# Kernel optimization log

Measured on AMD Instinct MI355X. Metric: run time of the kernel, lower is better.

The kernel has to match this reference:

```python
import jax, jax.numpy as jnp
import numpy as np

B, L, T, V = 32, 200, 500, 80
DM, DE = 256, 512
D4 = 4 * DM              # 1024 (decoder LSTM width)
R = 2                    # reduction rate
STEPS = T // R           # 250 decoder steps
KSIZE, PADC, NFILT, DA = 31, 15, 32, 128
ZONEOUT, KEEP = 0.1, 0.5
MAXSTEP = 500            # hard-coded attention buffer length


def setup_inputs() -> dict:
    key = jax.random.key(0)
    ks = jax.random.split(key, 24)
    def lin(k, fan_in, shape):
        s = 1.0 / np.sqrt(fan_in)
        return jax.random.uniform(k, shape, minval=-s, maxval=s, dtype=jnp.float32)
    return {
        'meltarget': jax.random.normal(ks[0], (B, T, V), jnp.float32),
        'e_outputs': jax.random.normal(ks[1], (B, L, DE), jnp.float32),
        'conv_w':    lin(ks[2], KSIZE, (NFILT, 1, KSIZE)),
        'W_convproj': lin(ks[3], NFILT, (NFILT, DA)),
        'W_encproj': lin(ks[4], DE, (DE, DA)), 'b_encproj': lin(ks[5], DE, (DA,)),
        'W_decproj': lin(ks[6], D4, (D4, DA)),
        'W_self':    lin(ks[7], DA, (DA,)),
        'W_pre1': lin(ks[8], V, (V, DM)),   'b_pre1': lin(ks[9], V, (DM,)),
        'W_pre2': lin(ks[10], DM, (DM, DM)), 'b_pre2': lin(ks[11], DM, (DM,)),
        'W_l1_ys': lin(ks[12], DM, (DM, 4 * D4)),
        'W_l1_ss': lin(ks[13], D4, (D4, 4 * D4)),
        'W_l1_gs': lin(ks[14], 2 * DM, (2 * DM, 4 * D4)), 'b_l1_gs': lin(ks[15], 2 * DM, (4 * D4,)),
        'W_l2_is': lin(ks[16], D4, (D4, 4 * D4)),
        'W_l2_ss': lin(ks[17], D4, (D4, 4 * D4)), 'b_l2_ss': lin(ks[18], D4, (4 * D4,)),
        'W_frame': lin(ks[19], D4 + 2 * DM, (D4 + 2 * DM, V * R)), 'b_frame': lin(ks[20], D4 + 2 * DM, (V * R,)),
        'W_token': lin(ks[21], D4 + 2 * DM, (D4 + 2 * DM, R)),     'b_token': lin(ks[22], D4 + 2 * DM, (R,)),
    }


def _gate(x):
    # tanh(x*0.5)*0.5 + 0.5 == sigmoid(x), kept in the original's form
    return jnp.tanh(x * 0.5) * 0.5 + 0.5


def reference(meltarget, e_outputs, conv_w, W_convproj, W_encproj, b_encproj,
              W_decproj, W_self, W_pre1, b_pre1, W_pre2, b_pre2,
              W_l1_ys, W_l1_ss, W_l1_gs, b_l1_gs, W_l2_is, W_l2_ss, b_l2_ss,
              W_frame, b_frame, W_token, b_token):
    base_key = jax.random.key(1234)
    encproj = e_outputs @ W_encproj + b_encproj              # [B,L,DA], step-invariant
    mel_last = jnp.transpose(meltarget[:, R - 1::R, :], (1, 0, 2))  # [STEPS,B,V]

    def step_fn(carry, xs):
        prev_pred, cum_alpha, s1, c1, s2, c2 = carry
        step, mel_t = xs
        kd1, kd2, kz1, kz2 = jax.random.split(jax.random.fold_in(base_key, step), 4)
        # location-sensitive attention
        ac = jax.lax.conv_general_dilated(
            cum_alpha[:, None, :], conv_w, (1,), [(PADC, PADC)],
            dimension_numbers=('NCH', 'OIH', 'NCH'))         # [B,32,L]
        attconv = jnp.einsum('bfl,fa->bla', ac, W_convproj)  # [B,L,DA]
        decproj = (s2 @ W_decproj)[:, None, :]               # [B,1,DA]
        e = jnp.tanh(decproj + encproj + attconv)
        score = e @ W_self                                   # [B,L]
        alpha = jax.nn.softmax(score, axis=1)
        cum_alpha = cum_alpha + alpha
        g = jnp.einsum('bl,bld->bd', alpha, e_outputs)       # [B,DE]
        # prenet with dropout p=0.5
        pre1 = jax.nn.relu(prev_pred @ W_pre1 + b_pre1)
        pre1 = pre1 * jax.random.bernoulli(kd1, KEEP, pre1.shape) / KEEP
        pre2 = jax.nn.relu(pre1 @ W_pre2 + b_pre2)
        pre2 = pre2 * jax.random.bernoulli(kd2, KEEP, pre2.shape) / KEEP
        # LSTM cell 1 with zoneout
        rec = pre2 @ W_l1_ys + s1 @ W_l1_ss + g @ W_l1_gs + b_l1_gs
        i1, f1, cg1, o1 = jnp.split(rec, 4, axis=1)
        m1 = jnp.floor(jax.random.uniform(kz1, (B, D4)) + ZONEOUT)  # Bernoulli(zoneout) keep-old mask
        c1n = m1 * c1 + (1.0 - m1) * (_gate(f1) * c1 + _gate(i1) * jnp.tanh(cg1))
        s1n = m1 * s1 + (1.0 - m1) * (_gate(o1) * jnp.tanh(c1n))
        # LSTM cell 2 with zoneout
        rec2 = s1n @ W_l2_is + s2 @ W_l2_ss + b_l2_ss
        i2, f2, cg2, o2 = jnp.split(rec2, 4, axis=1)
        m2 = jnp.floor(jax.random.uniform(kz2, (B, D4)) + ZONEOUT)
        c2n = m2 * c2 + (1.0 - m2) * (_gate(f2) * c2 + _gate(i2) * jnp.tanh(cg2))
        s2n = m2 * s2 + (1.0 - m2) * (_gate(o2) * jnp.tanh(c2n))
        proj_in = jnp.concatenate([s2n, g], axis=1)          # [B, D4+2*DM]
        frame = proj_in @ W_frame + b_frame                  # [B, R*V]
        token = proj_in @ W_token + b_token                  # [B, R]
        return (mel_t, cum_alpha, s1n, c1n, s2n, c2n), (frame, token, alpha)

    z = jnp.zeros((B, D4), jnp.float32)
    carry0 = (jnp.zeros((B, V), jnp.float32), jnp.zeros((B, L), jnp.float32), z, z, z, z)
    _, (frames, tokens, alphas) = jax.lax.scan(step_fn, carry0, (jnp.arange(STEPS), mel_last))
    frame_sent = jnp.transpose(frames, (1, 0, 2)).reshape(B, STEPS * R, V)
    token_sent = jnp.transpose(tokens, (1, 0, 2)).reshape(B, STEPS * R)
    attn = jnp.zeros((B, MAXSTEP, L), jnp.float32).at[:, :STEPS].set(
        jax.lax.stop_gradient(jnp.transpose(alphas, (1, 0, 2))))
    return frame_sent, token_sent, attn
```

## Files before the change

### kernel.cpp

```cpp
#include <hip/hip_runtime.h>
#include <cstdint>
#include <cstddef>


static constexpr int NSTEP = 250;

static constexpr size_t OFF_ENCPROJ = 0;
static constexpr size_t OFF_CWT     = 819200;
static constexpr size_t OFF_KEYS    = 823296;
static constexpr size_t OFF_PRE2    = 825344;
static constexpr size_t OFF_G       = 2873344;
static constexpr size_t OFF_S2      = 6969344;
static constexpr size_t OFF_S1      = 15194112;
static constexpr size_t OFF_C1      = 15259648;
static constexpr size_t OFF_C2      = 15292416;
static constexpr size_t OFF_CUM     = 15325184;
static constexpr size_t OFF_DPART   = 15333376;
static constexpr size_t OFF_SC      = 15366144;
static constexpr size_t OFF_P1      = 15390720;
static constexpr size_t OFF_P2      = 17225728;

static constexpr size_t OUT_TOK  = 1280000;
static constexpr size_t OUT_ATTN = 1296000;

__device__ __forceinline__ uint2 threefry(unsigned k0, unsigned k1, unsigned c0, unsigned c1) {
  unsigned ks2 = k0 ^ k1 ^ 0x1BD11BDAu;
  unsigned x0 = c0 + k0, x1 = c1 + k1;
#define TFR(rot) { x0 += x1; x1 = (x1 << (rot)) | (x1 >> (32 - (rot))); x1 ^= x0; }
  TFR(13) TFR(15) TFR(26) TFR(6)   x0 += k1;  x1 += ks2 + 1u;
  TFR(17) TFR(29) TFR(16) TFR(24)  x0 += ks2; x1 += k0 + 2u;
  TFR(13) TFR(15) TFR(26) TFR(6)   x0 += k0;  x1 += k1 + 3u;
  TFR(17) TFR(29) TFR(16) TFR(24)  x0 += k1;  x1 += ks2 + 4u;
  TFR(13) TFR(15) TFR(26) TFR(6)   x0 += ks2; x1 += k0 + 5u;
#undef TFR
  return make_uint2(x0, x1);
}

__device__ __forceinline__ float u32_to_uniform(unsigned b) {
  return __uint_as_float((b >> 9) | 0x3f800000u) - 1.0f;
}

__device__ __forceinline__ float rng_uniform(unsigned k0, unsigned k1, unsigned i) {
  uint2 h = threefry(k0, k1, 0u, i);
  return u32_to_uniform(h.x ^ h.y);
}

__device__ __forceinline__ float gatef(float x) { return tanhf(x * 0.5f) * 0.5f + 0.5f; }

#define FMA4(A, S, W) { (A).x = fmaf((S), (W).x, (A).x); (A).y = fmaf((S), (W).y, (A).y); \
                        (A).z = fmaf((S), (W).z, (A).z); (A).w = fmaf((S), (W).w, (A).w); }

__global__ __launch_bounds__(256) void k_init(float* __restrict__ ws, float* __restrict__ out,
                                              const float* __restrict__ conv_w,
                                              const float* __restrict__ Wcp) {
  const size_t NZERO1 = 172032;
  const size_t NZERO2 = 32768;
  const size_t NATTN  = 1600000;
  const size_t NKEYS  = 250;
  const size_t NCWT   = 4096;
  const size_t TOTAL  = NZERO1 + NZERO2 + NATTN + NKEYS + NCWT;
  unsigned* keys = (unsigned*)(ws + OFF_KEYS);
  for (size_t i = (size_t)blockIdx.x * 256 + threadIdx.x; i < TOTAL; i += (size_t)gridDim.x * 256) {
    if (i < NZERO1) {
      ws[OFF_S1 + i] = 0.f;
    } else if (i < NZERO1 + NZERO2) {
      ws[OFF_S2 + (i - NZERO1)] = 0.f;
    } else if (i < NZERO1 + NZERO2 + NATTN) {
      size_t r = i - NZERO1 - NZERO2;
      size_t b = r / 50000, rem = r % 50000;
      out[OUT_ATTN + b * 100000 + 50000 + rem] = 0.f;
    } else if (i < NZERO1 + NZERO2 + NATTN + NKEYS) {
      int s = (int)(i - NZERO1 - NZERO2 - NATTN);
      uint2 F = threefry(0u, 1234u, 0u, (unsigned)s);
      uint2 kd1 = threefry(F.x, F.y, 0u, 0u);
      uint2 kd2 = threefry(F.x, F.y, 0u, 1u);
      uint2 kz1 = threefry(F.x, F.y, 0u, 2u);
      uint2 kz2 = threefry(F.x, F.y, 0u, 3u);
      keys[s * 8 + 0] = kd1.x; keys[s * 8 + 1] = kd1.y;
      keys[s * 8 + 2] = kd2.x; keys[s * 8 + 3] = kd2.y;
      keys[s * 8 + 4] = kz1.x; keys[s * 8 + 5] = kz1.y;
      keys[s * 8 + 6] = kz2.x; keys[s * 8 + 7] = kz2.y;
    } else {
      size_t r = i - NZERO1 - NZERO2 - NATTN - NKEYS;
      int a = (int)(r >> 5), kk = (int)(r & 31);
      float v = 0.f;
      if (kk < 31) {
        for (int f = 0; f < 32; ++f) v = fmaf(conv_w[f * 31 + kk], Wcp[f * 128 + a], v);
      }
      ws[OFF_CWT + r] = v;
    }
  }
}

__global__ __launch_bounds__(256) void k_encproj(const float* __restrict__ e_out,
                                                 const float* __restrict__ Wenc,
                                                 const float* __restrict__ benc,
                                                 float* __restrict__ encproj) {
  __shared__ __align__(16) float xs[32 * 516];
  int t = threadIdx.x;
  int r0 = blockIdx.x * 32;
  for (int i = 0; i < 64; ++i) {
    int idx = t + 256 * i; int rb = idx >> 9, kk = idx & 511;
    xs[rb * 516 + kk] = e_out[(size_t)(r0 + rb) * 512 + kk];
  }
  __syncthreads();
  int a = t & 127, rh = t >> 7;
  float acc[16];
#pragma unroll
  for (int r = 0; r < 16; ++r) acc[r] = 0.f;
  const float4* xv = (const float4*)xs;
  for (int k4 = 0; k4 < 128; ++k4) {
    const float* wp = Wenc + (size_t)(k4 * 4) * 128 + a;
    float w0 = wp[0], w1 = wp[128], w2 = wp[256], w3 = wp[384];
#pragma unroll
    for (int r = 0; r < 16; ++r) {
      float4 x4 = xv[(rh * 16 + r) * 129 + k4];
      acc[r] = fmaf(x4.x, w0, acc[r]); acc[r] = fmaf(x4.y, w1, acc[r]);
      acc[r] = fmaf(x4.z, w2, acc[r]); acc[r] = fmaf(x4.w, w3, acc[r]);
    }
  }
  float bb = benc[a];
  for (int r = 0; r < 16; ++r)
    encproj[(size_t)(r0 + rh * 16 + r) * 128 + a] = acc[r] + bb;
}

__global__ __launch_bounds__(256) void k_prenet(const float* __restrict__ mel,
                                                const float* __restrict__ W1, const float* __restrict__ b1,
                                                const float* __restrict__ W2, const float* __restrict__ b2,
                                                const unsigned* __restrict__ keys,
                                                float* __restrict__ pre2_all) {
  int s = blockIdx.x, t = threadIdx.x;
  __shared__ __align__(16) float prev[32 * 80];
  __shared__ __align__(16) float p1[32 * 256];
  for (int i = 0; i < 10; ++i) {
    int idx = t + 256 * i;
    int bb = idx / 80, vv = idx % 80;
    prev[idx] = (s == 0) ? 0.f : mel[(size_t)bb * 40000 + (size_t)(2 * s - 1) * 80 + vv];
  }
  __syncthreads();
  unsigned kd10 = keys[s * 8 + 0], kd11 = keys[s * 8 + 1];
  unsigned kd20 = keys[s * 8 + 2], kd21 = keys[s * 8 + 3];
  float acc[32];
  float bias = b1[t];
#pragma unroll
  for (int b = 0; b < 32; ++b) acc[b] = bias;
  for (int k4 = 0; k4 < 20; ++k4) {
    const float* wp = W1 + (size_t)(k4 * 4) * 256 + t;
    float w0 = wp[0], w1 = wp[256], w2 = wp[512], w3 = wp[768];
#pragma unroll
    for (int b = 0; b < 32; ++b) {
      float4 x4 = *(const float4*)(prev + b * 80 + k4 * 4);
      acc[b] = fmaf(x4.x, w0, acc[b]); acc[b] = fmaf(x4.y, w1, acc[b]);
      acc[b] = fmaf(x4.z, w2, acc[b]); acc[b] = fmaf(x4.w, w3, acc[b]);
    }
  }
#pragma unroll
  for (int b = 0; b < 32; ++b) {
    float r = fmaxf(acc[b], 0.f);
    float u = rng_uniform(kd10, kd11, (unsigned)(b * 256 + t));
    p1[b * 256 + t] = (u < 0.5f) ? r * 2.f : 0.f;
  }
  __syncthreads();
  float bias2 = b2[t];
#pragma unroll
  for (int b = 0; b < 32; ++b) acc[b] = bias2;
  for (int k4 = 0; k4 < 64; ++k4) {
    const float* wp = W2 + (size_t)(k4 * 4) * 256 + t;
    float w0 = wp[0], w1 = wp[256], w2 = wp[512], w3 = wp[768];
#pragma unroll
    for (int b = 0; b < 32; ++b) {
      float4 x4 = *(const float4*)(p1 + b * 256 + k4 * 4);
      acc[b] = fmaf(x4.x, w0, acc[b]); acc[b] = fmaf(x4.y, w1, acc[b]);
      acc[b] = fmaf(x4.z, w2, acc[b]); acc[b] = fmaf(x4.w, w3, acc[b]);
    }
  }
  for (int b = 0; b < 32; ++b) {
    float r = fmaxf(acc[b], 0.f);
    float u = rng_uniform(kd20, kd21, (unsigned)(b * 256 + t));
    pre2_all[(size_t)(s * 32 + b) * 256 + t] = (u < 0.5f) ? r * 2.f : 0.f;
  }
}

__global__ __launch_bounds__(256) void k_escore(const float* __restrict__ dpart,
                                                const float* __restrict__ encproj,
                                                const float* __restrict__ cwt,
                                                const float* __restrict__ cum,
                                                const float* __restrict__ Wself,
                                                float* __restrict__ sglob) {
  int b = blockIdx.x & 31, p = blockIdx.x >> 5;
  int t = threadIdx.x;
  __shared__ float dp[128];
  __shared__ float ca[232];
  __shared__ float scpart[4];
  if (t < 128) {
    float acc = 0.f;
#pragma unroll
    for (int q = 0; q < 8; ++q) acc += dpart[(b * 8 + q) * 128 + t];
    dp[t] = acc;
  }
  if (t < 232) ca[t] = (t >= 15 && t < 215) ? cum[b * 200 + (t - 15)] : 0.f;
  __syncthreads();
  int a = t & 127, lh = t >> 7;
  float cwr[31];
#pragma unroll
  for (int k = 0; k < 31; ++k) cwr[k] = cwt[a * 32 + k];
  float wself = Wself[a];
  float dpr = dp[a];
  for (int ii = 0; ii < 13; ++ii) {
    int lo = ii * 2 + lh;
    int l = p * 25 + lo;
    float v = 0.f;
    if (lo < 25) {
      float conv = 0.f;
#pragma unroll
      for (int k = 0; k < 31; ++k) conv = fmaf(ca[l + k], cwr[k], conv);
      float e = tanhf(dpr + encproj[(size_t)(b * 200 + l) * 128 + a] + conv);
      v = e * wself;
    }
#pragma unroll
    for (int off = 32; off > 0; off >>= 1) v += __shfl_xor(v, off, 64);
    if ((t & 63) == 0) scpart[t >> 6] = v;
    __syncthreads();
    if (t == 0) sglob[b * 200 + p * 25 + ii * 2] = scpart[0] + scpart[1];
    if (t == 128 && ii < 12) sglob[b * 200 + p * 25 + ii * 2 + 1] = scpart[2] + scpart[3];
    __syncthreads();
  }
}

__global__ __launch_bounds__(256) void k_attng(const float* __restrict__ sglob,
                                               const float* __restrict__ e_out,
                                               float* __restrict__ cum,
                                               float* __restrict__ g_out,
                                               float* __restrict__ attn_out) {
  int b = blockIdx.x & 31, p = blockIdx.x >> 5;
  int t = threadIdx.x;
  __shared__ float sc[200];
  __shared__ float red[8];
  __shared__ float bcv[2];
  __shared__ float gpart[4][64];
  if (t < 200) sc[t] = sglob[b * 200 + t];
  __syncthreads();
  float v = (t < 200) ? sc[t] : -3.4e38f;
#pragma unroll
  for (int off = 32; off > 0; off >>= 1) v = fmaxf(v, __shfl_xor(v, off, 64));
  if ((t & 63) == 0) red[t >> 6] = v;
  __syncthreads();
  if (t == 0) bcv[0] = fmaxf(fmaxf(red[0], red[1]), fmaxf(red[2], red[3]));
  __syncthreads();
  float mx = bcv[0];
  float ex = (t < 200) ? expf(sc[t] - mx) : 0.f;
  float sv = ex;
#pragma unroll
  for (int off = 32; off > 0; off >>= 1) sv += __shfl_xor(sv, off, 64);
  if ((t & 63) == 0) red[4 + (t >> 6)] = sv;
  __syncthreads();
  if (t == 0) bcv[1] = (red[4] + red[5]) + (red[6] + red[7]);
  __syncthreads();
  float denom = bcv[1];
  if (t < 200) {
    float al = ex / denom;
    sc[t] = al;
    if (p == 0) {
      cum[b * 200 + t] += al;
      attn_out[(size_t)b * 100000 + t] = al;
    }
  }
  __syncthreads();
  int d = p * 64 + (t & 63), lq = t >> 6;
  const float* eb = e_out + (size_t)b * 102400 + d;
  float acc = 0.f;
  for (int l = lq * 50; l < lq * 50 + 50; ++l) acc = fmaf(sc[l], eb[(size_t)l * 512], acc);
  gpart[lq][t & 63] = acc;
  __syncthreads();
  if (t < 64)
    g_out[b * 512 + p * 64 + t] = (gpart[0][t] + gpart[1][t]) + (gpart[2][t] + gpart[3][t]);
}

__device__ __forceinline__ void gemm_body(
    const float* __restrict__ W0, int k0,
    float* __restrict__ part, int c, int jt,
    const float* __restrict__ xs ) {
  int t = threadIdx.x;
  int jq = t & 31, bq = t >> 5;
  int j = jt * 32 + jq;
  float4 acc[4];
  acc[0] = acc[1] = acc[2] = acc[3] = make_float4(0, 0, 0, 0);
  const float4* xv = (const float4*)xs;
  const float* Wb = W0 + (size_t)k0 * 4096 + j;
#pragma unroll 4
  for (int k4 = 0; k4 < 32; ++k4) {
    float4 xq[4];
    xq[0] = xv[(bq * 4 + 0) * 33 + k4];
    xq[1] = xv[(bq * 4 + 1) * 33 + k4];
    xq[2] = xv[(bq * 4 + 2) * 33 + k4];
    xq[3] = xv[(bq * 4 + 3) * 33 + k4];
    const float* wr = Wb + (size_t)(k4 * 4) * 4096;
#pragma unroll
    for (int ks = 0; ks < 4; ++ks) {
      float wi = wr[0], wf = wr[1024], wc = wr[2048], wo = wr[3072];
      wr += 4096;
#pragma unroll
      for (int r = 0; r < 4; ++r) {
        float xval = ((const float*)&xq[r])[ks];
        acc[r].x = fmaf(xval, wi, acc[r].x);
        acc[r].y = fmaf(xval, wf, acc[r].y);
        acc[r].z = fmaf(xval, wc, acc[r].z);
        acc[r].w = fmaf(xval, wo, acc[r].w);
      }
    }
  }
  float* pb = part + (size_t)c * 131072 + (size_t)(bq * 4) * 4096 + j;
#pragma unroll
  for (int r = 0; r < 4; ++r) {
    float* pr = pb + r * 4096;
    pr[0] = acc[r].x; pr[1024] = acc[r].y; pr[2048] = acc[r].z; pr[3072] = acc[r].w;
  }
}

__global__ __launch_bounds__(256) void k_b1g(
    const float* __restrict__ pre2_s, const float* __restrict__ s1old,
    const float* __restrict__ g_s,
    const float* __restrict__ Wys, const float* __restrict__ Wss, const float* __restrict__ Wgs,
    float* __restrict__ part) {
  int t = threadIdx.x;
  int jt = blockIdx.x & 31, c = blockIdx.x >> 5;
  __shared__ __align__(16) float xs[32 * 132];
  {
    int r = t >> 3, kq = t & 7;
    const float* src;
    if (c < 2)       src = pre2_s + r * 256 + c * 128;
    else if (c < 10) src = s1old + r * 1024 + (c - 2) * 128;
    else             src = g_s + r * 512 + (c - 10) * 128;
    const float4* s4 = (const float4*)(src + kq * 16);
    float4* d4 = (float4*)(xs + r * 132 + kq * 16);
    d4[0] = s4[0]; d4[1] = s4[1]; d4[2] = s4[2]; d4[3] = s4[3];
  }
  const float* W0; int k0;
  if (c < 2)       { W0 = Wys; k0 = c * 128; }
  else if (c < 10) { W0 = Wss; k0 = (c - 2) * 128; }
  else             { W0 = Wgs; k0 = (c - 10) * 128; }
  __syncthreads();
  gemm_body(W0, k0, part, c, jt, xs);
}

__global__ __launch_bounds__(256) void k_b2g(
    const float* __restrict__ s1new, const float* __restrict__ s2prev,
    const float* __restrict__ Wis, const float* __restrict__ Wss2,
    float* __restrict__ part) {
  int t = threadIdx.x;
  int jt = blockIdx.x & 31, c = blockIdx.x >> 5;
  __shared__ __align__(16) float xs[32 * 132];
  {
    int r = t >> 3, kq = t & 7;
    const float* src = (c < 8) ? (s1new + r * 1024 + c * 128)
                               : (s2prev + r * 1024 + (c - 8) * 128);
    const float4* s4 = (const float4*)(src + kq * 16);
    float4* d4 = (float4*)(xs + r * 132 + kq * 16);
    d4[0] = s4[0]; d4[1] = s4[1]; d4[2] = s4[2]; d4[3] = s4[3];
  }
  const float* W0; int k0;
  if (c < 8) { W0 = Wis;  k0 = c * 128; }
  else       { W0 = Wss2; k0 = (c - 8) * 128; }
  __syncthreads();
  gemm_body(W0, k0, part, c, jt, xs);
}

__global__ __launch_bounds__(256) void k_cell1(
    const float* __restrict__ part, const float* __restrict__ bias,
    const float* __restrict__ sold, float* __restrict__ snew, float* __restrict__ cst,
    const unsigned* __restrict__ keyp) {
  int e = blockIdx.x * 256 + threadIdx.x;
  int b = e >> 10, j = e & 1023;
  float gi = bias[j], gf = bias[1024 + j], gc = bias[2048 + j], go = bias[3072 + j];
  const float* pc = part + (size_t)b * 4096 + j;
#pragma unroll
  for (int cc = 0; cc < 14; ++cc) {
    const float* p2 = pc + (size_t)cc * 131072;
    gi += p2[0]; gf += p2[1024]; gc += p2[2048]; go += p2[3072];
  }
  float u = rng_uniform(keyp[0], keyp[1], (unsigned)e);
  float m = floorf(u + 0.1f);
  float co = cst[e], so = sold[e];
  float cn = fmaf(gatef(gf), co, gatef(gi) * tanhf(gc));
  float cnew = (m > 0.5f) ? co : cn;
  float sn = (m > 0.5f) ? so : (gatef(go) * tanhf(cnew));
  cst[e] = cnew;
  snew[e] = sn;
}

__global__ __launch_bounds__(256) void k_cell2dp(
    const float* __restrict__ part, const float* __restrict__ bias,
    const float* __restrict__ sold, float* __restrict__ snew, float* __restrict__ cst,
    const unsigned* __restrict__ keyp,
    const float* __restrict__ Wdec, float* __restrict__ dpart) {
  int b = blockIdx.x & 31, p = blockIdx.x >> 5;
  int t = threadIdx.x;
  __shared__ float s2l[128];
  __shared__ float dtmp[256];
  if (t < 128) {
    int j = p * 128 + t;
    int e = b * 1024 + j;
    float gi = bias[j], gf = bias[1024 + j], gc = bias[2048 + j], go = bias[3072 + j];
    const float* pc = part + (size_t)b * 4096 + j;
#pragma unroll
    for (int cc = 0; cc < 16; ++cc) {
      const float* p2 = pc + (size_t)cc * 131072;
      gi += p2[0]; gf += p2[1024]; gc += p2[2048]; go += p2[3072];
    }
    float u = rng_uniform(keyp[0], keyp[1], (unsigned)e);
    float m = floorf(u + 0.1f);
    float co = cst[e], so = sold[e];
    float cn = fmaf(gatef(gf), co, gatef(gi) * tanhf(gc));
    float cnew = (m > 0.5f) ? co : cn;
    float sn = (m > 0.5f) ? so : (gatef(go) * tanhf(cnew));
    cst[e] = cnew;
    snew[e] = sn;
    s2l[t] = sn;
  }
  __syncthreads();
  int a = t & 127, h = t >> 7;
  const float* wp = Wdec + (size_t)(p * 128 + h * 64) * 128 + a;
  float acc = 0.f;
#pragma unroll 8
  for (int r = 0; r < 64; ++r) acc = fmaf(s2l[h * 64 + r], wp[(size_t)r * 128], acc);
  dtmp[t] = acc;
  __syncthreads();
  if (t < 128) dpart[(b * 8 + p) * 128 + t] = dtmp[t] + dtmp[t + 128];
}

__global__ __launch_bounds__(256) void k_frame(const float* __restrict__ s2_all,
                                               const float* __restrict__ g_all,
                                               const float* __restrict__ Wf,
                                               const float* __restrict__ bf,
                                               const float* __restrict__ Wt,
                                               const float* __restrict__ bt,
                                               float* __restrict__ out_frame,
                                               float* __restrict__ out_tok) {
  int s = blockIdx.x, t = threadIdx.x;
  __shared__ __align__(16) float xs[32 * 516];
  int b = t >> 3, ci = t & 7;
  int tb = t >> 1, tr = t & 1;
  float4 acc[5];
#pragma unroll
  for (int r = 0; r < 5; ++r) acc[r] = make_float4(0, 0, 0, 0);
  float tok = 0.f;
  for (int ch = 0; ch < 3; ++ch) {
    for (int i = 0; i < 64; ++i) {
      int idx = t + 256 * i;
      int rb = idx >> 9, kk = idx & 511;
      float vsrc = (ch < 2) ? s2_all[(size_t)(s + 1) * 32768 + rb * 1024 + ch * 512 + kk]
                            : g_all[(size_t)s * 16384 + rb * 512 + kk];
      xs[rb * 516 + kk] = vsrc;
    }
    __syncthreads();
    const float4* xv = (const float4*)xs;
    for (int k4 = 0; k4 < 128; ++k4) {
      float4 x4 = xv[b * 129 + k4];
      int kglob = ch * 512 + k4 * 4;
#pragma unroll
      for (int rep = 0; rep < 5; ++rep) {
        int c4 = ci * 4 + rep * 32;
        const float* wrow = Wf + (size_t)kglob * 160 + c4;
        float4 w0 = *(const float4*)(wrow);
        float4 w1 = *(const float4*)(wrow + 160);
        float4 w2 = *(const float4*)(wrow + 320);
        float4 w3 = *(const float4*)(wrow + 480);
        FMA4(acc[rep], x4.x, w0); FMA4(acc[rep], x4.y, w1);
        FMA4(acc[rep], x4.z, w2); FMA4(acc[rep], x4.w, w3);
      }
      if (t < 64) {
        float4 xt = xv[tb * 129 + k4];
        tok = fmaf(xt.x, Wt[(size_t)(kglob + 0) * 2 + tr], tok);
        tok = fmaf(xt.y, Wt[(size_t)(kglob + 1) * 2 + tr], tok);
        tok = fmaf(xt.z, Wt[(size_t)(kglob + 2) * 2 + tr], tok);
        tok = fmaf(xt.w, Wt[(size_t)(kglob + 3) * 2 + tr], tok);
      }
    }
    __syncthreads();
  }
#pragma unroll
  for (int rep = 0; rep < 5; ++rep) {
    float vals[4] = {acc[rep].x, acc[rep].y, acc[rep].z, acc[rep].w};
#pragma unroll
    for (int jj = 0; jj < 4; ++jj) {
      int cc = ci * 4 + rep * 32 + jj;
      float val = vals[jj] + bf[cc];
      int row = 2 * s + (cc >= 80 ? 1 : 0);
      int col = cc - (cc >= 80 ? 80 : 0);
      out_frame[(size_t)b * 40000 + (size_t)row * 80 + col] = val;
    }
  }
  if (t < 64) out_tok[(size_t)tb * 500 + 2 * s + tr] = tok + bt[tr];
}

extern "C" void kernel_launch(void* const* d_in, const int* in_sizes, int n_in,
                              void* d_out_v, int out_size, void* d_ws, size_t ws_size,
                              hipStream_t stream) {
  (void)in_sizes; (void)n_in; (void)out_size; (void)ws_size;
  const float* mel      = (const float*)d_in[0];
  const float* e_out    = (const float*)d_in[1];
  const float* conv_w   = (const float*)d_in[2];
  const float* Wcp      = (const float*)d_in[3];
  const float* Wenc     = (const float*)d_in[4];
  const float* benc     = (const float*)d_in[5];
  const float* Wdec     = (const float*)d_in[6];
  const float* Wself    = (const float*)d_in[7];
  const float* Wp1      = (const float*)d_in[8];
  const float* bp1      = (const float*)d_in[9];
  const float* Wp2      = (const float*)d_in[10];
  const float* bp2      = (const float*)d_in[11];
  const float* Wys      = (const float*)d_in[12];
  const float* Wss      = (const float*)d_in[13];
  const float* Wgs      = (const float*)d_in[14];
  const float* bgs      = (const float*)d_in[15];
  const float* Wis      = (const float*)d_in[16];
  const float* Wss2     = (const float*)d_in[17];
  const float* bss2     = (const float*)d_in[18];
  const float* Wf       = (const float*)d_in[19];
  const float* bf       = (const float*)d_in[20];
  const float* Wt       = (const float*)d_in[21];
  const float* bt       = (const float*)d_in[22];
  float* ws  = (float*)d_ws;
  float* out = (float*)d_out_v;
  const unsigned* keys = (const unsigned*)(ws + OFF_KEYS);

  hipLaunchKernelGGL(k_init, dim3(1024), dim3(256), 0, stream, ws, out, conv_w, Wcp);
  hipLaunchKernelGGL(k_encproj, dim3(200), dim3(256), 0, stream, e_out, Wenc, benc, ws + OFF_ENCPROJ);
  hipLaunchKernelGGL(k_prenet, dim3(250), dim3(256), 0, stream, mel, Wp1, bp1, Wp2, bp2, keys, ws + OFF_PRE2);

  for (int s = 0; s < NSTEP; ++s) {
    float* s1old = ws + OFF_S1 + (size_t)(s & 1) * 32768;
    float* s1new = ws + OFF_S1 + (size_t)((s + 1) & 1) * 32768;
    float* s2s   = ws + OFF_S2 + (size_t)s * 32768;
    float* s2n   = ws + OFF_S2 + (size_t)(s + 1) * 32768;
    float* gs    = ws + OFF_G  + (size_t)s * 16384;
    hipLaunchKernelGGL(k_escore, dim3(256), dim3(256), 0, stream,
                       ws + OFF_DPART, ws + OFF_ENCPROJ, ws + OFF_CWT, ws + OFF_CUM,
                       Wself, ws + OFF_SC);
    hipLaunchKernelGGL(k_attng, dim3(256), dim3(256), 0, stream,
                       ws + OFF_SC, e_out, ws + OFF_CUM, gs,
                       out + OUT_ATTN + (size_t)s * 200);
    hipLaunchKernelGGL(k_b1g, dim3(448), dim3(256), 0, stream,
                       ws + OFF_PRE2 + (size_t)s * 8192, s1old, gs, Wys, Wss, Wgs,
                       ws + OFF_P1);
    hipLaunchKernelGGL(k_cell1, dim3(128), dim3(256), 0, stream,
                       ws + OFF_P1, bgs, s1old, s1new, ws + OFF_C1, keys + s * 8 + 4);
    hipLaunchKernelGGL(k_b2g, dim3(512), dim3(256), 0, stream,
                       s1new, s2s, Wis, Wss2, ws + OFF_P2);
    hipLaunchKernelGGL(k_cell2dp, dim3(256), dim3(256), 0, stream,
                       ws + OFF_P2, bss2, s2s, s2n, ws + OFF_C2, keys + s * 8 + 6,
                       Wdec, ws + OFF_DPART);
  }
  hipLaunchKernelGGL(k_frame, dim3(250), dim3(256), 0, stream,
                     ws + OFF_S2, ws + OFF_G, Wf, bf, Wt, bt, out, out + OUT_TOK);
}
```

Before: 15.50 ms.

## Fuse LSTM2 cell, decoder projection, scores, softmax and context into one kernel

Merges the second LSTM cell update, the decoder-state projection, the location-aware energy scores, the softmax and the context reduction into a single per-batch 1024-thread kernel. This cuts the per-step launch count from six to four and removes global round trips for dpart and the score buffer. The cell-2 update of step s moves to the start of step s+1, with a separate final kernel for the last step. In exchange each step now uses only 32 large blocks, which lowers parallelism for the attention work.

```diff
diff --git a/kernel.cpp b/kernel.cpp
--- a/kernel.cpp
+++ b/kernel.cpp
@@ -15,8 +15,6 @@
 static constexpr size_t OFF_C1      = 15259648;
 static constexpr size_t OFF_C2      = 15292416;
 static constexpr size_t OFF_CUM     = 15325184;
-static constexpr size_t OFF_DPART   = 15333376;
-static constexpr size_t OFF_SC      = 15366144;
 static constexpr size_t OFF_P1      = 15390720;
 static constexpr size_t OFF_P2      = 17225728;
 
@@ -53,7 +51,7 @@
 __global__ __launch_bounds__(256) void k_init(float* __restrict__ ws, float* __restrict__ out,
                                               const float* __restrict__ conv_w,
                                               const float* __restrict__ Wcp) {
-  const size_t NZERO1 = 172032;
+  const size_t NZERO1 = 139264;
   const size_t NZERO2 = 32768;
   const size_t NATTN  = 1600000;
   const size_t NKEYS  = 250;
@@ -181,99 +179,144 @@
   }
 }
 
-__global__ __launch_bounds__(256) void k_escore(const float* __restrict__ dpart,
-                                                const float* __restrict__ encproj,
-                                                const float* __restrict__ cwt,
-                                                const float* __restrict__ cum,
-                                                const float* __restrict__ Wself,
-                                                float* __restrict__ sglob) {
-  int b = blockIdx.x & 31, p = blockIdx.x >> 5;
-  int t = threadIdx.x;
-  __shared__ float dp[128];
+__global__ __launch_bounds__(1024) void k_att(
+    int s,
+    const float* __restrict__ part,
+    const float* __restrict__ bias2,
+    const float* __restrict__ s2old,
+    float* __restrict__ s2new,
+    float* __restrict__ c2,
+    const unsigned* __restrict__ keys,
+    const float* __restrict__ Wdec,
+    const float* __restrict__ encproj,
+    const float* __restrict__ cwt,
+    float* __restrict__ cum,
+    const float* __restrict__ Wself,
+    const float* __restrict__ e_out,
+    float* __restrict__ g_out,
+    float* __restrict__ attn_out) {
+  int b = blockIdx.x, t = threadIdx.x;
+  __shared__ float s2l[1024];
+  __shared__ float dpp[8][128];
+  __shared__ float dpf[128];
   __shared__ float ca[232];
-  __shared__ float scpart[4];
+  __shared__ float red[25][16];
+  __shared__ float sc[200];
+  __shared__ float redm[16];
+  __shared__ float bcv[2];
+  __shared__ float gpart[2][512];
+
+  if (s > 0) {
+    int j = t, e = b * 1024 + j;
+    float gi = bias2[j], gf = bias2[1024 + j], gc = bias2[2048 + j], go = bias2[3072 + j];
+    const float* pc = part + (size_t)b * 4096 + j;
+#pragma unroll
+    for (int cc = 0; cc < 16; ++cc) {
+      const float* p2 = pc + (size_t)cc * 131072;
+      gi += p2[0]; gf += p2[1024]; gc += p2[2048]; go += p2[3072];
+    }
+    const unsigned* keyp = keys + (size_t)(s - 1) * 8 + 6;
+    float u = rng_uniform(keyp[0], keyp[1], (unsigned)e);
+    float m = floorf(u + 0.1f);
+    float co = c2[e], so = s2old[e];
+    float cn = fmaf(gatef(gf), co, gatef(gi) * tanhf(gc));
+    float cnew = (m > 0.5f) ? co : cn;
+    float sn = (m > 0.5f) ? so : (gatef(go) * tanhf(cnew));
+    c2[e] = cnew;
+    s2new[e] = sn;
+    s2l[j] = sn;
+  } else {
+    s2l[t] = 0.f;
+  }
+  __syncthreads();
+
+  {
+    int jg = t >> 7, a = t & 127;
+    const float* wp = Wdec + (size_t)(jg * 128) * 128 + a;
+    float a0 = 0.f, a1 = 0.f;
+#pragma unroll 8
+    for (int r = 0; r < 64; ++r) a0 = fmaf(s2l[jg * 128 + r], wp[(size_t)r * 128], a0);
+#pragma unroll 8
+    for (int r = 64; r < 128; ++r) a1 = fmaf(s2l[jg * 128 + r], wp[(size_t)r * 128], a1);
+    dpp[jg][a] = a0 + a1;
+  }
+  __syncthreads();
   if (t < 128) {
-    float acc = 0.f;
-#pragma unroll
-    for (int q = 0; q < 8; ++q) acc += dpart[(b * 8 + q) * 128 + t];
-    dp[t] = acc;
-  }
-  if (t < 232) ca[t] = (t >= 15 && t < 215) ? cum[b * 200 + (t - 15)] : 0.f;
-  __syncthreads();
-  int a = t & 127, lh = t >> 7;
-  float cwr[31];
-#pragma unroll
-  for (int k = 0; k < 31; ++k) cwr[k] = cwt[a * 32 + k];
-  float wself = Wself[a];
-  float dpr = dp[a];
-  for (int ii = 0; ii < 13; ++ii) {
-    int lo = ii * 2 + lh;
-    int l = p * 25 + lo;
     float v = 0.f;
-    if (lo < 25) {
+#pragma unroll
+    for (int q = 0; q < 8; ++q) v += dpp[q][t];
+    dpf[t] = v;
+  } else if (t < 360) {
+    int tt = t - 128;
+    ca[tt] = (tt >= 15 && tt < 215) ? cum[b * 200 + (tt - 15)] : 0.f;
+  }
+  __syncthreads();
+
+  {
+    int lg = t >> 7, a = t & 127;
+    float cwr[31];
+#pragma unroll
+    for (int k = 0; k < 31; ++k) cwr[k] = cwt[a * 32 + k];
+    float wself = Wself[a];
+    float dpr = dpf[a];
+    for (int i = 0; i < 25; ++i) {
+      int l = i * 8 + lg;
       float conv = 0.f;
 #pragma unroll
       for (int k = 0; k < 31; ++k) conv = fmaf(ca[l + k], cwr[k], conv);
       float e = tanhf(dpr + encproj[(size_t)(b * 200 + l) * 128 + a] + conv);
-      v = e * wself;
-    }
-#pragma unroll
-    for (int off = 32; off > 0; off >>= 1) v += __shfl_xor(v, off, 64);
-    if ((t & 63) == 0) scpart[t >> 6] = v;
-    __syncthreads();
-    if (t == 0) sglob[b * 200 + p * 25 + ii * 2] = scpart[0] + scpart[1];
-    if (t == 128 && ii < 12) sglob[b * 200 + p * 25 + ii * 2 + 1] = scpart[2] + scpart[3];
-    __syncthreads();
-  }
-}
-
-__global__ __launch_bounds__(256) void k_attng(const float* __restrict__ sglob,
-                                               const float* __restrict__ e_out,
-                                               float* __restrict__ cum,
-                                               float* __restrict__ g_out,
-                                               float* __restrict__ attn_out) {
-  int b = blockIdx.x & 31, p = blockIdx.x >> 5;
-  int t = threadIdx.x;
-  __shared__ float sc[200];
-  __shared__ float red[8];
-  __shared__ float bcv[2];
-  __shared__ float gpart[4][64];
-  if (t < 200) sc[t] = sglob[b * 200 + t];
-  __syncthreads();
-  float v = (t < 200) ? sc[t] : -3.4e38f;
-#pragma unroll
-  for (int off = 32; off > 0; off >>= 1) v = fmaxf(v, __shfl_xor(v, off, 64));
-  if ((t & 63) == 0) red[t >> 6] = v;
-  __syncthreads();
-  if (t == 0) bcv[0] = fmaxf(fmaxf(red[0], red[1]), fmaxf(red[2], red[3]));
+      float v = e * wself;
+#pragma unroll
+      for (int off = 32; off > 0; off >>= 1) v += __shfl_xor(v, off, 64);
+      if ((t & 63) == 0) red[i][t >> 6] = v;
+    }
+  }
+  __syncthreads();
+  if (t < 200) {
+    int i = t >> 3, lg2 = t & 7;
+    sc[t] = red[i][lg2 * 2] + red[i][lg2 * 2 + 1];
+  }
+  __syncthreads();
+
+  {
+    float v = (t < 200) ? sc[t] : -3.4e38f;
+#pragma unroll
+    for (int off = 32; off > 0; off >>= 1) v = fmaxf(v, __shfl_xor(v, off, 64));
+    if ((t & 63) == 0) redm[t >> 6] = v;
+  }
+  __syncthreads();
+  if (t == 0) bcv[0] = fmaxf(fmaxf(redm[0], redm[1]), fmaxf(redm[2], redm[3]));
   __syncthreads();
   float mx = bcv[0];
   float ex = (t < 200) ? expf(sc[t] - mx) : 0.f;
-  float sv = ex;
-#pragma unroll
-  for (int off = 32; off > 0; off >>= 1) sv += __shfl_xor(sv, off, 64);
-  if ((t & 63) == 0) red[4 + (t >> 6)] = sv;
-  __syncthreads();
-  if (t == 0) bcv[1] = (red[4] + red[5]) + (red[6] + red[7]);
+  {
+    float sv = ex;
+#pragma unroll
+    for (int off = 32; off > 0; off >>= 1) sv += __shfl_xor(sv, off, 64);
+    if ((t & 63) == 0) redm[t >> 6] = sv;
+  }
+  __syncthreads();
+  if (t == 0) bcv[1] = (redm[0] + redm[1]) + (redm[2] + redm[3]);
   __syncthreads();
   float denom = bcv[1];
   if (t < 200) {
     float al = ex / denom;
     sc[t] = al;
-    if (p == 0) {
-      cum[b * 200 + t] += al;
-      attn_out[(size_t)b * 100000 + t] = al;
-    }
-  }
-  __syncthreads();
-  int d = p * 64 + (t & 63), lq = t >> 6;
-  const float* eb = e_out + (size_t)b * 102400 + d;
-  float acc = 0.f;
-  for (int l = lq * 50; l < lq * 50 + 50; ++l) acc = fmaf(sc[l], eb[(size_t)l * 512], acc);
-  gpart[lq][t & 63] = acc;
-  __syncthreads();
-  if (t < 64)
-    g_out[b * 512 + p * 64 + t] = (gpart[0][t] + gpart[1][t]) + (gpart[2][t] + gpart[3][t]);
+    cum[b * 200 + t] += al;
+    attn_out[(size_t)b * 100000 + t] = al;
+  }
+  __syncthreads();
+
+  {
+    int h = t >> 9, d = t & 511;
+    const float* eb = e_out + (size_t)b * 102400 + d;
+    float pa = 0.f, pb = 0.f;
+    for (int l = h * 100; l < h * 100 + 50; ++l) pa = fmaf(sc[l], eb[(size_t)l * 512], pa);
+    for (int l = h * 100 + 50; l < h * 100 + 100; ++l) pb = fmaf(sc[l], eb[(size_t)l * 512], pb);
+    gpart[h][d] = pa + pb;
+  }
+  __syncthreads();
+  if (t < 512) g_out[b * 512 + t] = gpart[0][t] + gpart[1][t];
 }
 
 __device__ __forceinline__ void gemm_body(
@@ -388,44 +431,27 @@
   snew[e] = sn;
 }
 
-__global__ __launch_bounds__(256) void k_cell2dp(
+__global__ __launch_bounds__(256) void k_cellfin(
     const float* __restrict__ part, const float* __restrict__ bias,
     const float* __restrict__ sold, float* __restrict__ snew, float* __restrict__ cst,
-    const unsigned* __restrict__ keyp,
-    const float* __restrict__ Wdec, float* __restrict__ dpart) {
-  int b = blockIdx.x & 31, p = blockIdx.x >> 5;
-  int t = threadIdx.x;
-  __shared__ float s2l[128];
-  __shared__ float dtmp[256];
-  if (t < 128) {
-    int j = p * 128 + t;
-    int e = b * 1024 + j;
-    float gi = bias[j], gf = bias[1024 + j], gc = bias[2048 + j], go = bias[3072 + j];
-    const float* pc = part + (size_t)b * 4096 + j;
-#pragma unroll
-    for (int cc = 0; cc < 16; ++cc) {
-      const float* p2 = pc + (size_t)cc * 131072;
-      gi += p2[0]; gf += p2[1024]; gc += p2[2048]; go += p2[3072];
-    }
-    float u = rng_uniform(keyp[0], keyp[1], (unsigned)e);
-    float m = floorf(u + 0.1f);
-    float co = cst[e], so = sold[e];
-    float cn = fmaf(gatef(gf), co, gatef(gi) * tanhf(gc));
-    float cnew = (m > 0.5f) ? co : cn;
-    float sn = (m > 0.5f) ? so : (gatef(go) * tanhf(cnew));
-    cst[e] = cnew;
-    snew[e] = sn;
-    s2l[t] = sn;
-  }
-  __syncthreads();
-  int a = t & 127, h = t >> 7;
-  const float* wp = Wdec + (size_t)(p * 128 + h * 64) * 128 + a;
-  float acc = 0.f;
-#pragma unroll 8
-  for (int r = 0; r < 64; ++r) acc = fmaf(s2l[h * 64 + r], wp[(size_t)r * 128], acc);
-  dtmp[t] = acc;
-  __syncthreads();
-  if (t < 128) dpart[(b * 8 + p) * 128 + t] = dtmp[t] + dtmp[t + 128];
+    const unsigned* __restrict__ keyp) {
+  int e = blockIdx.x * 256 + threadIdx.x;
+  int b = e >> 10, j = e & 1023;
+  float gi = bias[j], gf = bias[1024 + j], gc = bias[2048 + j], go = bias[3072 + j];
+  const float* pc = part + (size_t)b * 4096 + j;
+#pragma unroll
+  for (int cc = 0; cc < 16; ++cc) {
+    const float* p2 = pc + (size_t)cc * 131072;
+    gi += p2[0]; gf += p2[1024]; gc += p2[2048]; go += p2[3072];
+  }
+  float u = rng_uniform(keyp[0], keyp[1], (unsigned)e);
+  float m = floorf(u + 0.1f);
+  float co = cst[e], so = sold[e];
+  float cn = fmaf(gatef(gf), co, gatef(gi) * tanhf(gc));
+  float cnew = (m > 0.5f) ? co : cn;
+  float sn = (m > 0.5f) ? so : (gatef(go) * tanhf(cnew));
+  cst[e] = cnew;
+  snew[e] = sn;
 }
 
 __global__ __launch_bounds__(256) void k_frame(const float* __restrict__ s2_all,
@@ -531,26 +557,25 @@
   for (int s = 0; s < NSTEP; ++s) {
     float* s1old = ws + OFF_S1 + (size_t)(s & 1) * 32768;
     float* s1new = ws + OFF_S1 + (size_t)((s + 1) & 1) * 32768;
-    float* s2s   = ws + OFF_S2 + (size_t)s * 32768;
-    float* s2n   = ws + OFF_S2 + (size_t)(s + 1) * 32768;
+    float* s2old = ws + OFF_S2 + (size_t)(s > 0 ? s - 1 : 0) * 32768;
+    float* s2cur = ws + OFF_S2 + (size_t)s * 32768;
     float* gs    = ws + OFF_G  + (size_t)s * 16384;
-    hipLaunchKernelGGL(k_escore, dim3(256), dim3(256), 0, stream,
-                       ws + OFF_DPART, ws + OFF_ENCPROJ, ws + OFF_CWT, ws + OFF_CUM,
-                       Wself, ws + OFF_SC);
-    hipLaunchKernelGGL(k_attng, dim3(256), dim3(256), 0, stream,
-                       ws + OFF_SC, e_out, ws + OFF_CUM, gs,
-                       out + OUT_ATTN + (size_t)s * 200);
+    hipLaunchKernelGGL(k_att, dim3(32), dim3(1024), 0, stream,
+                       s, ws + OFF_P2, bss2, s2old, s2cur, ws + OFF_C2,
+                       (const unsigned*)(ws + OFF_KEYS), Wdec,
+                       ws + OFF_ENCPROJ, ws + OFF_CWT, ws + OFF_CUM, Wself,
+                       e_out, gs, out + OUT_ATTN + (size_t)s * 200);
     hipLaunchKernelGGL(k_b1g, dim3(448), dim3(256), 0, stream,
                        ws + OFF_PRE2 + (size_t)s * 8192, s1old, gs, Wys, Wss, Wgs,
                        ws + OFF_P1);
     hipLaunchKernelGGL(k_cell1, dim3(128), dim3(256), 0, stream,
                        ws + OFF_P1, bgs, s1old, s1new, ws + OFF_C1, keys + s * 8 + 4);
     hipLaunchKernelGGL(k_b2g, dim3(512), dim3(256), 0, stream,
-                       s1new, s2s, Wis, Wss2, ws + OFF_P2);
-    hipLaunchKernelGGL(k_cell2dp, dim3(256), dim3(256), 0, stream,
-                       ws + OFF_P2, bss2, s2s, s2n, ws + OFF_C2, keys + s * 8 + 6,
-                       Wdec, ws + OFF_DPART);
-  }
+                       s1new, s2cur, Wis, Wss2, ws + OFF_P2);
+  }
+  hipLaunchKernelGGL(k_cellfin, dim3(128), dim3(256), 0, stream,
+                     ws + OFF_P2, bss2, ws + OFF_S2 + (size_t)249 * 32768,
+                     ws + OFF_S2 + (size_t)250 * 32768, ws + OFF_C2, keys + 249 * 8 + 6);
   hipLaunchKernelGGL(k_frame, dim3(250), dim3(256), 0, stream,
                      ws + OFF_S2, ws + OFF_G, Wf, bf, Wt, bt, out, out + OUT_TOK);
 }
```

Result: slower. 19.41 ms (+25.2%).

## Fuse LSTM gate GEMMs with cell updates and move decoder projection into escore

Applied to the files above, without the earlier changes.

Each LSTM layer's split-K gate GEMM plus its separate cell kernel are merged into one kernel per layer. Each block now owns 4 hidden columns across all four gates, loops over the full K range and applies the zoneout cell update in-block, so the partial-sum buffers and their reduction pass are gone. The decoder attention projection (s2 @ W_decproj) is recomputed inside k_escore from s2, removing the dpart workspace. This cuts per-step launches from six to four and avoids round trips through global memory. In exchange, each fused GEMM runs with fewer blocks (256 instead of 448/512) and has less K parallelism per block, and every escore block redundantly recomputes the 1024x128 projection for its batch row.

```diff
diff --git a/kernel.cpp b/kernel.cpp
--- a/kernel.cpp
+++ b/kernel.cpp
@@ -15,10 +15,7 @@
 static constexpr size_t OFF_C1      = 15259648;
 static constexpr size_t OFF_C2      = 15292416;
 static constexpr size_t OFF_CUM     = 15325184;
-static constexpr size_t OFF_DPART   = 15333376;
 static constexpr size_t OFF_SC      = 15366144;
-static constexpr size_t OFF_P1      = 15390720;
-static constexpr size_t OFF_P2      = 17225728;
 
 static constexpr size_t OUT_TOK  = 1280000;
 static constexpr size_t OUT_ATTN = 1296000;
@@ -53,7 +50,7 @@
 __global__ __launch_bounds__(256) void k_init(float* __restrict__ ws, float* __restrict__ out,
                                               const float* __restrict__ conv_w,
                                               const float* __restrict__ Wcp) {
-  const size_t NZERO1 = 172032;
+  const size_t NZERO1 = 139264;
   const size_t NZERO2 = 32768;
   const size_t NATTN  = 1600000;
   const size_t NKEYS  = 250;
@@ -181,7 +178,8 @@
   }
 }
 
-__global__ __launch_bounds__(256) void k_escore(const float* __restrict__ dpart,
+__global__ __launch_bounds__(256) void k_escore(const float* __restrict__ s2g,
+                                                const float* __restrict__ Wdec,
                                                 const float* __restrict__ encproj,
                                                 const float* __restrict__ cwt,
                                                 const float* __restrict__ cum,
@@ -189,16 +187,26 @@
                                                 float* __restrict__ sglob) {
   int b = blockIdx.x & 31, p = blockIdx.x >> 5;
   int t = threadIdx.x;
+  __shared__ float s2l[1024];
   __shared__ float dp[128];
   __shared__ float ca[232];
   __shared__ float scpart[4];
+  for (int i = t; i < 1024; i += 256) s2l[i] = s2g[b * 1024 + i];
+  if (t < 232) ca[t] = (t >= 15 && t < 215) ? cum[b * 200 + (t - 15)] : 0.f;
+  __syncthreads();
   if (t < 128) {
     float acc = 0.f;
-#pragma unroll
-    for (int q = 0; q < 8; ++q) acc += dpart[(b * 8 + q) * 128 + t];
+    for (int q = 0; q < 8; ++q) {
+      const float* wp = Wdec + (size_t)(q * 128) * 128 + t;
+      float a0 = 0.f, a1 = 0.f;
+#pragma unroll 8
+      for (int r = 0; r < 64; ++r) a0 = fmaf(s2l[q * 128 + r], wp[(size_t)r * 128], a0);
+#pragma unroll 8
+      for (int r = 64; r < 128; ++r) a1 = fmaf(s2l[q * 128 + r], wp[(size_t)r * 128], a1);
+      acc += a0 + a1;
+    }
     dp[t] = acc;
   }
-  if (t < 232) ca[t] = (t >= 15 && t < 215) ? cum[b * 200 + (t - 15)] : 0.f;
   __syncthreads();
   int a = t & 127, lh = t >> 7;
   float cwr[31];
@@ -276,156 +284,130 @@
     g_out[b * 512 + p * 64 + t] = (gpart[0][t] + gpart[1][t]) + (gpart[2][t] + gpart[3][t]);
 }
 
-__device__ __forceinline__ void gemm_body(
-    const float* __restrict__ W0, int k0,
-    float* __restrict__ part, int c, int jt,
-    const float* __restrict__ xs ) {
-  int t = threadIdx.x;
-  int jq = t & 31, bq = t >> 5;
-  int j = jt * 32 + jq;
-  float4 acc[4];
-  acc[0] = acc[1] = acc[2] = acc[3] = make_float4(0, 0, 0, 0);
-  const float4* xv = (const float4*)xs;
-  const float* Wb = W0 + (size_t)k0 * 4096 + j;
-#pragma unroll 4
-  for (int k4 = 0; k4 < 32; ++k4) {
-    float4 xq[4];
-    xq[0] = xv[(bq * 4 + 0) * 33 + k4];
-    xq[1] = xv[(bq * 4 + 1) * 33 + k4];
-    xq[2] = xv[(bq * 4 + 2) * 33 + k4];
-    xq[3] = xv[(bq * 4 + 3) * 33 + k4];
-    const float* wr = Wb + (size_t)(k4 * 4) * 4096;
-#pragma unroll
-    for (int ks = 0; ks < 4; ++ks) {
-      float wi = wr[0], wf = wr[1024], wc = wr[2048], wo = wr[3072];
-      wr += 4096;
-#pragma unroll
-      for (int r = 0; r < 4; ++r) {
-        float xval = ((const float*)&xq[r])[ks];
-        acc[r].x = fmaf(xval, wi, acc[r].x);
-        acc[r].y = fmaf(xval, wf, acc[r].y);
-        acc[r].z = fmaf(xval, wc, acc[r].z);
-        acc[r].w = fmaf(xval, wo, acc[r].w);
-      }
-    }
-  }
-  float* pb = part + (size_t)c * 131072 + (size_t)(bq * 4) * 4096 + j;
-#pragma unroll
-  for (int r = 0; r < 4; ++r) {
-    float* pr = pb + r * 4096;
-    pr[0] = acc[r].x; pr[1024] = acc[r].y; pr[2048] = acc[r].z; pr[3072] = acc[r].w;
-  }
-}
-
-__global__ __launch_bounds__(256) void k_b1g(
+__global__ __launch_bounds__(256) void k_b1f(
     const float* __restrict__ pre2_s, const float* __restrict__ s1old,
     const float* __restrict__ g_s,
     const float* __restrict__ Wys, const float* __restrict__ Wss, const float* __restrict__ Wgs,
-    float* __restrict__ part) {
-  int t = threadIdx.x;
-  int jt = blockIdx.x & 31, c = blockIdx.x >> 5;
+    const float* __restrict__ bias, float* __restrict__ snew, float* __restrict__ cst,
+    const unsigned* __restrict__ keyp) {
   __shared__ __align__(16) float xs[32 * 132];
-  {
-    int r = t >> 3, kq = t & 7;
-    const float* src;
-    if (c < 2)       src = pre2_s + r * 256 + c * 128;
-    else if (c < 10) src = s1old + r * 1024 + (c - 2) * 128;
-    else             src = g_s + r * 512 + (c - 10) * 128;
-    const float4* s4 = (const float4*)(src + kq * 16);
-    float4* d4 = (float4*)(xs + r * 132 + kq * 16);
-    d4[0] = s4[0]; d4[1] = s4[1]; d4[2] = s4[2]; d4[3] = s4[3];
-  }
-  const float* W0; int k0;
-  if (c < 2)       { W0 = Wys; k0 = c * 128; }
-  else if (c < 10) { W0 = Wss; k0 = (c - 2) * 128; }
-  else             { W0 = Wgs; k0 = (c - 10) * 128; }
-  __syncthreads();
-  gemm_body(W0, k0, part, c, jt, xs);
-}
-
-__global__ __launch_bounds__(256) void k_b2g(
-    const float* __restrict__ s1new, const float* __restrict__ s2prev,
-    const float* __restrict__ Wis, const float* __restrict__ Wss2,
-    float* __restrict__ part) {
-  int t = threadIdx.x;
-  int jt = blockIdx.x & 31, c = blockIdx.x >> 5;
-  __shared__ __align__(16) float xs[32 * 132];
-  {
-    int r = t >> 3, kq = t & 7;
-    const float* src = (c < 8) ? (s1new + r * 1024 + c * 128)
-                               : (s2prev + r * 1024 + (c - 8) * 128);
-    const float4* s4 = (const float4*)(src + kq * 16);
-    float4* d4 = (float4*)(xs + r * 132 + kq * 16);
-    d4[0] = s4[0]; d4[1] = s4[1]; d4[2] = s4[2]; d4[3] = s4[3];
-  }
-  const float* W0; int k0;
-  if (c < 8) { W0 = Wis;  k0 = c * 128; }
-  else       { W0 = Wss2; k0 = (c - 8) * 128; }
-  __syncthreads();
-  gemm_body(W0, k0, part, c, jt, xs);
-}
-
-__global__ __launch_bounds__(256) void k_cell1(
-    const float* __restrict__ part, const float* __restrict__ bias,
-    const float* __restrict__ sold, float* __restrict__ snew, float* __restrict__ cst,
-    const unsigned* __restrict__ keyp) {
-  int e = blockIdx.x * 256 + threadIdx.x;
-  int b = e >> 10, j = e & 1023;
-  float gi = bias[j], gf = bias[1024 + j], gc = bias[2048 + j], go = bias[3072 + j];
-  const float* pc = part + (size_t)b * 4096 + j;
-#pragma unroll
+  __shared__ float gl[32][16];
+  int t = threadIdx.x, jt = blockIdx.x;
+  int col = t & 15, bq = t >> 4;
+  int g = col >> 2, jj = col & 3;
+  int b0 = bq * 2, b1 = b0 + 1;
+  int jcol = g * 1024 + jt * 4 + jj;
+  float v0 = bias[jcol], v1 = v0;
   for (int cc = 0; cc < 14; ++cc) {
-    const float* p2 = pc + (size_t)cc * 131072;
-    gi += p2[0]; gf += p2[1024]; gc += p2[2048]; go += p2[3072];
-  }
-  float u = rng_uniform(keyp[0], keyp[1], (unsigned)e);
-  float m = floorf(u + 0.1f);
-  float co = cst[e], so = sold[e];
-  float cn = fmaf(gatef(gf), co, gatef(gi) * tanhf(gc));
-  float cnew = (m > 0.5f) ? co : cn;
-  float sn = (m > 0.5f) ? so : (gatef(go) * tanhf(cnew));
-  cst[e] = cnew;
-  snew[e] = sn;
-}
-
-__global__ __launch_bounds__(256) void k_cell2dp(
-    const float* __restrict__ part, const float* __restrict__ bias,
-    const float* __restrict__ sold, float* __restrict__ snew, float* __restrict__ cst,
-    const unsigned* __restrict__ keyp,
-    const float* __restrict__ Wdec, float* __restrict__ dpart) {
-  int b = blockIdx.x & 31, p = blockIdx.x >> 5;
-  int t = threadIdx.x;
-  __shared__ float s2l[128];
-  __shared__ float dtmp[256];
+    __syncthreads();
+    {
+      int r = t >> 3, kq = t & 7;
+      const float* src;
+      if (cc < 2)       src = pre2_s + r * 256 + cc * 128;
+      else if (cc < 10) src = s1old + r * 1024 + (cc - 2) * 128;
+      else              src = g_s + r * 512 + (cc - 10) * 128;
+      const float4* s4 = (const float4*)(src + kq * 16);
+      float4* d4 = (float4*)(xs + r * 132 + kq * 16);
+      d4[0] = s4[0]; d4[1] = s4[1]; d4[2] = s4[2]; d4[3] = s4[3];
+    }
+    __syncthreads();
+    const float* W0; int k0;
+    if (cc < 2)       { W0 = Wys; k0 = cc * 128; }
+    else if (cc < 10) { W0 = Wss; k0 = (cc - 2) * 128; }
+    else              { W0 = Wgs; k0 = (cc - 10) * 128; }
+    const float* wp = W0 + (size_t)k0 * 4096 + jcol;
+    const float4* x0 = (const float4*)(xs + b0 * 132);
+    const float4* x1 = (const float4*)(xs + b1 * 132);
+    float p0 = 0.f, p1 = 0.f;
+#pragma unroll 8
+    for (int k4 = 0; k4 < 32; ++k4) {
+      float4 a0 = x0[k4], a1 = x1[k4];
+      const float* wk = wp + (size_t)(k4 * 4) * 4096;
+      float w0 = wk[0], w1 = wk[4096], w2 = wk[8192], w3 = wk[12288];
+      p0 = fmaf(a0.x, w0, p0); p1 = fmaf(a1.x, w0, p1);
+      p0 = fmaf(a0.y, w1, p0); p1 = fmaf(a1.y, w1, p1);
+      p0 = fmaf(a0.z, w2, p0); p1 = fmaf(a1.z, w2, p1);
+      p0 = fmaf(a0.w, w3, p0); p1 = fmaf(a1.w, w3, p1);
+    }
+    v0 += p0; v1 += p1;
+  }
+  gl[b0][col] = v0; gl[b1][col] = v1;
+  __syncthreads();
   if (t < 128) {
-    int j = p * 128 + t;
+    int b = t >> 2, j4 = t & 3;
+    int j = jt * 4 + j4;
     int e = b * 1024 + j;
-    float gi = bias[j], gf = bias[1024 + j], gc = bias[2048 + j], go = bias[3072 + j];
-    const float* pc = part + (size_t)b * 4096 + j;
-#pragma unroll
-    for (int cc = 0; cc < 16; ++cc) {
-      const float* p2 = pc + (size_t)cc * 131072;
-      gi += p2[0]; gf += p2[1024]; gc += p2[2048]; go += p2[3072];
-    }
+    float gi = gl[b][j4], gf = gl[b][4 + j4], gc = gl[b][8 + j4], go = gl[b][12 + j4];
     float u = rng_uniform(keyp[0], keyp[1], (unsigned)e);
     float m = floorf(u + 0.1f);
-    float co = cst[e], so = sold[e];
+    float co = cst[e], so = s1old[e];
     float cn = fmaf(gatef(gf), co, gatef(gi) * tanhf(gc));
     float cnew = (m > 0.5f) ? co : cn;
     float sn = (m > 0.5f) ? so : (gatef(go) * tanhf(cnew));
     cst[e] = cnew;
     snew[e] = sn;
-    s2l[t] = sn;
-  }
-  __syncthreads();
-  int a = t & 127, h = t >> 7;
-  const float* wp = Wdec + (size_t)(p * 128 + h * 64) * 128 + a;
-  float acc = 0.f;
+  }
+}
+
+__global__ __launch_bounds__(256) void k_b2f(
+    const float* __restrict__ s1new, const float* __restrict__ s2prev,
+    const float* __restrict__ Wis, const float* __restrict__ Wss2,
+    const float* __restrict__ bias, float* __restrict__ snew, float* __restrict__ cst,
+    const unsigned* __restrict__ keyp) {
+  __shared__ __align__(16) float xs[32 * 132];
+  __shared__ float gl[32][16];
+  int t = threadIdx.x, jt = blockIdx.x;
+  int col = t & 15, bq = t >> 4;
+  int g = col >> 2, jj = col & 3;
+  int b0 = bq * 2, b1 = b0 + 1;
+  int jcol = g * 1024 + jt * 4 + jj;
+  float v0 = bias[jcol], v1 = v0;
+  for (int cc = 0; cc < 16; ++cc) {
+    __syncthreads();
+    {
+      int r = t >> 3, kq = t & 7;
+      const float* src = (cc < 8) ? (s1new + r * 1024 + cc * 128)
+                                  : (s2prev + r * 1024 + (cc - 8) * 128);
+      const float4* s4 = (const float4*)(src + kq * 16);
+      float4* d4 = (float4*)(xs + r * 132 + kq * 16);
+      d4[0] = s4[0]; d4[1] = s4[1]; d4[2] = s4[2]; d4[3] = s4[3];
+    }
+    __syncthreads();
+    const float* W0; int k0;
+    if (cc < 8) { W0 = Wis;  k0 = cc * 128; }
+    else        { W0 = Wss2; k0 = (cc - 8) * 128; }
+    const float* wp = W0 + (size_t)k0 * 4096 + jcol;
+    const float4* x0 = (const float4*)(xs + b0 * 132);
+    const float4* x1 = (const float4*)(xs + b1 * 132);
+    float p0 = 0.f, p1 = 0.f;
 #pragma unroll 8
-  for (int r = 0; r < 64; ++r) acc = fmaf(s2l[h * 64 + r], wp[(size_t)r * 128], acc);
-  dtmp[t] = acc;
-  __syncthreads();
-  if (t < 128) dpart[(b * 8 + p) * 128 + t] = dtmp[t] + dtmp[t + 128];
+    for (int k4 = 0; k4 < 32; ++k4) {
+      float4 a0 = x0[k4], a1 = x1[k4];
+      const float* wk = wp + (size_t)(k4 * 4) * 4096;
+      float w0 = wk[0], w1 = wk[4096], w2 = wk[8192], w3 = wk[12288];
+      p0 = fmaf(a0.x, w0, p0); p1 = fmaf(a1.x, w0, p1);
+      p0 = fmaf(a0.y, w1, p0); p1 = fmaf(a1.y, w1, p1);
+      p0 = fmaf(a0.z, w2, p0); p1 = fmaf(a1.z, w2, p1);
+      p0 = fmaf(a0.w, w3, p0); p1 = fmaf(a1.w, w3, p1);
+    }
+    v0 += p0; v1 += p1;
+  }
+  gl[b0][col] = v0; gl[b1][col] = v1;
+  __syncthreads();
+  if (t < 128) {
+    int b = t >> 2, j4 = t & 3;
+    int j = jt * 4 + j4;
+    int e = b * 1024 + j;
+    float gi = gl[b][j4], gf = gl[b][4 + j4], gc = gl[b][8 + j4], go = gl[b][12 + j4];
+    float u = rng_uniform(keyp[0], keyp[1], (unsigned)e);
+    float m = floorf(u + 0.1f);
+    float co = cst[e], so = s2prev[e];
+    float cn = fmaf(gatef(gf), co, gatef(gi) * tanhf(gc));
+    float cnew = (m > 0.5f) ? co : cn;
+    float sn = (m > 0.5f) ? so : (gatef(go) * tanhf(cnew));
+    cst[e] = cnew;
+    snew[e] = sn;
+  }
 }
 
 __global__ __launch_bounds__(256) void k_frame(const float* __restrict__ s2_all,
@@ -535,21 +517,17 @@
     float* s2n   = ws + OFF_S2 + (size_t)(s + 1) * 32768;
     float* gs    = ws + OFF_G  + (size_t)s * 16384;
     hipLaunchKernelGGL(k_escore, dim3(256), dim3(256), 0, stream,
-                       ws + OFF_DPART, ws + OFF_ENCPROJ, ws + OFF_CWT, ws + OFF_CUM,
+                       s2s, Wdec, ws + OFF_ENCPROJ, ws + OFF_CWT, ws + OFF_CUM,
                        Wself, ws + OFF_SC);
     hipLaunchKernelGGL(k_attng, dim3(256), dim3(256), 0, stream,
                        ws + OFF_SC, e_out, ws + OFF_CUM, gs,
                        out + OUT_ATTN + (size_t)s * 200);
-    hipLaunchKernelGGL(k_b1g, dim3(448), dim3(256), 0, stream,
+    hipLaunchKernelGGL(k_b1f, dim3(256), dim3(256), 0, stream,
                        ws + OFF_PRE2 + (size_t)s * 8192, s1old, gs, Wys, Wss, Wgs,
-                       ws + OFF_P1);
-    hipLaunchKernelGGL(k_cell1, dim3(128), dim3(256), 0, stream,
-                       ws + OFF_P1, bgs, s1old, s1new, ws + OFF_C1, keys + s * 8 + 4);
-    hipLaunchKernelGGL(k_b2g, dim3(512), dim3(256), 0, stream,
-                       s1new, s2s, Wis, Wss2, ws + OFF_P2);
-    hipLaunchKernelGGL(k_cell2dp, dim3(256), dim3(256), 0, stream,
-                       ws + OFF_P2, bss2, s2s, s2n, ws + OFF_C2, keys + s * 8 + 6,
-                       Wdec, ws + OFF_DPART);
+                       bgs, s1new, ws + OFF_C1, keys + s * 8 + 4);
+    hipLaunchKernelGGL(k_b2f, dim3(256), dim3(256), 0, stream,
+                       s1new, s2s, Wis, Wss2,
+                       bss2, s2n, ws + OFF_C2, keys + s * 8 + 6);
   }
   hipLaunchKernelGGL(k_frame, dim3(250), dim3(256), 0, stream,
                      ws + OFF_S2, ws + OFF_G, Wf, bf, Wt, bt, out, out + OUT_TOK);
```

Result: slower. 58.94 ms (+280.2%).
